# Kernel tuning notes

Hardware: AMD Instinct MI355X
Metric: run time of the kernel (lower is better)

The kernel has to match this reference:

```python
import jax, jax.numpy as jnp
import numpy as np

EPS = 1e-5


def _layer_norm(x, gamma, beta):
    mu = jnp.mean(x, axis=-1, keepdims=True)
    var = jnp.var(x, axis=-1, keepdims=True)
    return (x - mu) * jax.lax.rsqrt(var + EPS) * gamma + beta


def setup_inputs() -> dict:
    key = jax.random.key(0)
    B, I, H = 4096, 1024, 1024
    ks = jax.random.split(key, 6)
    x = jax.random.normal(ks[0], (B, I), dtype=jnp.float32)
    h = jax.random.normal(ks[1], (B, H), dtype=jnp.float32)
    c = jax.random.normal(ks[2], (B, H), dtype=jnp.float32)
    # nn.Linear(I+H, 4H): weight [4H, I+H], bias [4H]
    bound = 1.0 / np.sqrt(I + H)
    W = jax.random.uniform(ks[3], (4 * H, I + H), minval=-bound, maxval=bound, dtype=jnp.float32)
    b = jax.random.uniform(ks[4], (4 * H,), minval=-bound, maxval=bound, dtype=jnp.float32)
    inp = {"x": x, "h": h, "c": c, "W": W, "b": b}
    for name in ("i", "f", "g", "o", "c"):
        inp[f"ln_{name}_g"] = jnp.ones((H,), dtype=jnp.float32)
        inp[f"ln_{name}_b"] = jnp.zeros((H,), dtype=jnp.float32)
    return inp


def reference(x, h, c, W, b, ln_i_g, ln_i_b, ln_f_g, ln_f_b, ln_g_g, ln_g_b,
              ln_o_g, ln_o_b, ln_c_g, ln_c_b):
    H = h.shape[-1]
    xh = jnp.concatenate([x, h], axis=-1)              # [B, I+H]
    gates = xh @ W.T + b                               # [B, 4H]
    i_raw, f_raw, g_raw, o_raw = jnp.split(gates, 4, axis=-1)
    i = jax.nn.sigmoid(_layer_norm(i_raw, ln_i_g, ln_i_b))
    f = jax.nn.sigmoid(_layer_norm(f_raw, ln_f_g, ln_f_b))
    g = jnp.tanh(_layer_norm(g_raw, ln_g_g, ln_g_b))
    o = jax.nn.sigmoid(_layer_norm(o_raw, ln_o_g, ln_o_b))
    c_new = f * c + i * g
    h_new = o * jnp.tanh(_layer_norm(c_new, ln_c_g, ln_c_b))
    return (h_new, c_new)
```

## Files before the change

kernel.cpp:

```cpp
#include <hip/hip_runtime.h>
#include <hip/hip_bf16.h>

#define B_ROWS 4096
#define H_DIM  1024
#define K_DIM  2048
#define N_DIM  4096
#define NT32   64

typedef __attribute__((ext_vector_type(8))) short bf16x8;
typedef __attribute__((ext_vector_type(16))) float f32x16;

__device__ __forceinline__ unsigned short f2bf(float f) {
  union { float f; unsigned int u; } v; v.f = f;
  unsigned int u = v.u;
  return (unsigned short)((u + 0x7fffu + ((u >> 16) & 1u)) >> 16);
}
__device__ __forceinline__ float bf2f(unsigned short u) {
  union { unsigned int u; float f; } v; v.u = ((unsigned int)u) << 16;
  return v.f;
}

__device__ __forceinline__ void gload_lds16(const void* g, void* l) {
  __builtin_amdgcn_global_load_lds(
      (const __attribute__((address_space(1))) void*)g,
      (__attribute__((address_space(3))) void*)l, 16, 0, 0);
}

__global__ __launch_bounds__(256) void pack_kernel(
    const float* __restrict__ x, const float* __restrict__ h,
    const float* __restrict__ W, unsigned short* __restrict__ Abf,
    unsigned short* __restrict__ Wbf) {
  int bid = blockIdx.x;
  if (bid < 8192) {
    int t = bid * 256 + threadIdx.x;
    int e = t * 4;
    int row = e >> 11;
    int col = e & 2047;
    const float* src = (col < 1024) ? (x + (size_t)row * 1024 + col)
                                    : (h + (size_t)row * 1024 + (col - 1024));
    float4 v = *(const float4*)src;
    ushort4 o;
    o.x = f2bf(v.x); o.y = f2bf(v.y); o.z = f2bf(v.z); o.w = f2bf(v.w);
    *(ushort4*)(Abf + e) = o;
  } else {
    int t = (bid - 8192) * 256 + threadIdx.x;
    int e = t * 4;
    float4 v = *(const float4*)(W + e);
    ushort4 o;
    o.x = f2bf(v.x); o.y = f2bf(v.y); o.z = f2bf(v.z); o.w = f2bf(v.w);
    *(ushort4*)(Wbf + e) = o;
  }
}


#define UNR _Pragma("unroll")

#define PSTG(kt, BUFOFS)                                                     \
  {                                                                          \
    const size_t ko = (size_t)(kt) << 5;                                     \
    char* const Ld = lds + (BUFOFS);                                         \
    gload_lds16(gAw0 + ko, Ld + dstOfs);                                     \
    gload_lds16(gAw1 + ko, Ld + dstOfs + 1024);                              \
    gload_lds16(gBw0 + ko, Ld + 16384 + dstOfs);                             \
    gload_lds16(gBw1 + ko, Ld + 16384 + dstOfs + 1024);                      \
  }

#define TILE1(tt, BUF, FRa, FRb, FWa, FWb)                                   \
  {                                                                          \
    const int kt3 = ((tt) + 3) & (NT32 - 1);                                 \
    PSTG(kt3, (((BUF) + 3) & 3) * 32768);                                    \
    asm volatile("s_waitcnt vmcnt(8)" ::: "memory");                         \
    __builtin_amdgcn_s_barrier();                                            \
    const char* const Ln = lds + (((BUF) + 1) & 3) * 32768;                  \
    UNR for (int R = 0; R < 4; ++R) {                                        \
      FWa[R][0] = *(const bf16x8*)(Ln + (wm * 8 + 2 * R) * 1024 + lofs0);    \
      FWa[R][1] = *(const bf16x8*)(Ln + (wm * 8 + 2 * R) * 1024 + lofs1);    \
    }                                                                        \
    UNR for (int ni = 0; ni < 2; ++ni) {                                     \
      FWb[ni][0] = *(const bf16x8*)(Ln + 16384 +                             \
                                    (wn * 4 + 2 * ni) * 1024 + lofs0);       \
      FWb[ni][1] = *(const bf16x8*)(Ln + 16384 +                             \
                                    (wn * 4 + 2 * ni) * 1024 + lofs1);       \
    }                                                                        \
    asm volatile("s_waitcnt lgkmcnt(12)" ::: "memory");                      \
    __builtin_amdgcn_sched_barrier(0);                                       \
    __builtin_amdgcn_s_setprio(1);                                           \
    UNR for (int R = 0; R < 4; ++R)                                          \
      UNR for (int ni = 0; ni < 2; ++ni)                                     \
        UNR for (int h = 0; h < 2; ++h)                                      \
          acc[R][ni] = __builtin_amdgcn_mfma_f32_32x32x16_bf16(              \
              FRa[R][h], FRb[ni][h], acc[R][ni], 0, 0, 0);                   \
    __builtin_amdgcn_s_setprio(0);                                           \
  }

__global__ __launch_bounds__(512, 2) void gemm_kernel(
    const unsigned short* __restrict__ A, const unsigned short* __restrict__ W,
    const float* __restrict__ bias, unsigned short* __restrict__ C) {
  __shared__ __align__(16) char lds[131072];

  const int tid = threadIdx.x;
  const int w = tid >> 6, l = tid & 63;
  const int wm = w >> 2, wn = w & 3;

  const int bid = blockIdx.x;
  const int xcd = bid & 7, li = bid >> 3;
  const int by = (xcd & 3) * 4 + (li >> 3);
  const int bx = ((xcd >> 2) << 3) + (li & 7);
  const int bm = by * 256, bn = bx * 256;

  const int lofs0 = ((l >> 4) & 1) * 1024 + (l & 15) * 64 +
                    ((((l >> 5) * 16) ^ ((l & 8) << 2)) ^ (((l >> 4) & 1) << 4));
  const int lofs1 = lofs0 ^ 32;

  const int lane_r = (l >> 2) & 15;
  const int lane_c0 = ((l & 3) * 8) ^ (((l >> 5) & 1) * 16);
  const int lane_c1 = lane_c0 ^ 8;

  const int dstOfs = w * 2048;
  const unsigned short* gAw0 = A + (size_t)(bm + 32 * w + lane_r) * K_DIM + lane_c0;
  const unsigned short* gAw1 = A + (size_t)(bm + 32 * w + 16 + lane_r) * K_DIM + lane_c1;
  const unsigned short* gBw0 = W + (size_t)(bn + 32 * w + lane_r) * K_DIM + lane_c0;
  const unsigned short* gBw1 = W + (size_t)(bn + 32 * w + 16 + lane_r) * K_DIM + lane_c1;

  f32x16 acc[4][2];
#pragma unroll
  for (int i = 0; i < 4; ++i)
#pragma unroll
    for (int j = 0; j < 2; ++j) acc[i][j] = (f32x16)0.0f;

  PSTG(0, 0);
  PSTG(1, 32768);
  PSTG(2, 65536);
  asm volatile("s_waitcnt vmcnt(8)" ::: "memory");
  __builtin_amdgcn_s_barrier();

  bf16x8 aP[4][2], bP[2][2], aQ[4][2], bQ[2][2];
#pragma unroll
  for (int R = 0; R < 4; ++R) {
    aP[R][0] = *(const bf16x8*)(lds + (wm * 8 + 2 * R) * 1024 + lofs0);
    aP[R][1] = *(const bf16x8*)(lds + (wm * 8 + 2 * R) * 1024 + lofs1);
  }
#pragma unroll
  for (int ni = 0; ni < 2; ++ni) {
    bP[ni][0] = *(const bf16x8*)(lds + 16384 + (wn * 4 + 2 * ni) * 1024 + lofs0);
    bP[ni][1] = *(const bf16x8*)(lds + 16384 + (wn * 4 + 2 * ni) * 1024 + lofs1);
  }

  for (int t = 0; t < NT32; t += 4) {
    TILE1(t + 0, 0, aP, bP, aQ, bQ);
    TILE1(t + 1, 1, aQ, bQ, aP, bP);
    TILE1(t + 2, 2, aP, bP, aQ, bQ);
    TILE1(t + 3, 3, aQ, bQ, aP, bP);
  }

  const int cl = l & 31, hi = l >> 5;
  float bv[2];
#pragma unroll
  for (int ni = 0; ni < 2; ++ni) bv[ni] = bias[bn + wn * 64 + ni * 32 + cl];
  unsigned short* Cb = C + (size_t)(bm + wm * 128) * N_DIM + bn + wn * 64;
#pragma unroll
  for (int R = 0; R < 4; ++R)
#pragma unroll
    for (int ni = 0; ni < 2; ++ni)
#pragma unroll
      for (int r = 0; r < 16; ++r) {
        const int row = R * 32 + (r & 3) + 8 * (r >> 2) + 4 * hi;
        Cb[(size_t)row * N_DIM + ni * 32 + cl] = f2bf(acc[R][ni][r] + bv[ni]);
      }
}

__device__ __forceinline__ float sigmoidf_(float x) {
  return 1.0f / (1.0f + __expf(-x));
}
__device__ __forceinline__ float tanhf_(float x) {
  return 1.0f - 2.0f / (__expf(2.0f * x) + 1.0f);
}

__global__ __launch_bounds__(256) void ln_lstm_kernel(
    const unsigned short* __restrict__ gates, const float* __restrict__ cprev,
    const float* __restrict__ g_i, const float* __restrict__ b_i,
    const float* __restrict__ g_f, const float* __restrict__ b_f,
    const float* __restrict__ g_g, const float* __restrict__ b_g,
    const float* __restrict__ g_o, const float* __restrict__ b_o,
    const float* __restrict__ g_c, const float* __restrict__ b_c,
    float* __restrict__ out) {
  const int b = blockIdx.x;
  const int t = threadIdx.x;
  const int wid = t >> 6, lane = t & 63;
  __shared__ float red[32];

  const unsigned short* grow = gates + (size_t)b * N_DIM;
  const int c0 = t * 4;

  float v[4][4];
#pragma unroll
  for (int g = 0; g < 4; g++) {
    ushort4 raw = *(const ushort4*)(grow + g * 1024 + c0);
    v[g][0] = bf2f(raw.x); v[g][1] = bf2f(raw.y);
    v[g][2] = bf2f(raw.z); v[g][3] = bf2f(raw.w);
  }

  const float4 gamma[4] = {*(const float4*)(g_i + c0), *(const float4*)(g_f + c0),
                           *(const float4*)(g_g + c0), *(const float4*)(g_o + c0)};
  const float4 beta[4]  = {*(const float4*)(b_i + c0), *(const float4*)(b_f + c0),
                           *(const float4*)(b_g + c0), *(const float4*)(b_o + c0)};

  float s[8];
#pragma unroll
  for (int g = 0; g < 4; g++) {
    s[g]     = v[g][0] + v[g][1] + v[g][2] + v[g][3];
    s[4 + g] = v[g][0]*v[g][0] + v[g][1]*v[g][1] + v[g][2]*v[g][2] + v[g][3]*v[g][3];
  }
#pragma unroll
  for (int o = 32; o >= 1; o >>= 1)
#pragma unroll
    for (int i = 0; i < 8; i++) s[i] += __shfl_xor(s[i], o, 64);
  if (lane == 0) {
#pragma unroll
    for (int i = 0; i < 8; i++) red[wid * 8 + i] = s[i];
  }
  __syncthreads();
#pragma unroll
  for (int i = 0; i < 8; i++) s[i] = red[i] + red[8 + i] + red[16 + i] + red[24 + i];

  float a[4][4];
#pragma unroll
  for (int g = 0; g < 4; g++) {
    float mu = s[g] * (1.0f / 1024.0f);
    float var = s[4 + g] * (1.0f / 1024.0f) - mu * mu;
    float inv = rsqrtf(var + 1e-5f);
    const float* gm = (const float*)&gamma[g];
    const float* bt = (const float*)&beta[g];
#pragma unroll
    for (int j = 0; j < 4; j++) {
      float n = (v[g][j] - mu) * inv * gm[j] + bt[j];
      a[g][j] = (g == 2) ? tanhf_(n) : sigmoidf_(n);
    }
  }

  float4 cp = *(const float4*)(cprev + (size_t)b * 1024 + c0);
  const float* cpe = (const float*)&cp;
  float cn[4];
#pragma unroll
  for (int j = 0; j < 4; j++)
    cn[j] = a[1][j] * cpe[j] + a[0][j] * a[2][j];

  {
    float u0 = cn[0] + cn[1] + cn[2] + cn[3];
    float u1 = cn[0]*cn[0] + cn[1]*cn[1] + cn[2]*cn[2] + cn[3]*cn[3];
#pragma unroll
    for (int o = 32; o >= 1; o >>= 1) {
      u0 += __shfl_xor(u0, o, 64);
      u1 += __shfl_xor(u1, o, 64);
    }
    __syncthreads();
    if (lane == 0) { red[wid * 2] = u0; red[wid * 2 + 1] = u1; }
    __syncthreads();
    u0 = red[0] + red[2] + red[4] + red[6];
    u1 = red[1] + red[3] + red[5] + red[7];
    float mu = u0 * (1.0f / 1024.0f);
    float var = u1 * (1.0f / 1024.0f) - mu * mu;
    float inv = rsqrtf(var + 1e-5f);
    float4 gm = *(const float4*)(g_c + c0);
    float4 bt = *(const float4*)(b_c + c0);
    const float* gme = (const float*)&gm;
    const float* bte = (const float*)&bt;
    float hn[4];
#pragma unroll
    for (int j = 0; j < 4; j++) {
      float n = (cn[j] - mu) * inv * gme[j] + bte[j];
      hn[j] = a[3][j] * tanhf_(n);
    }
    *(float4*)(out + (size_t)b * 1024 + c0) = make_float4(hn[0], hn[1], hn[2], hn[3]);
    *(float4*)(out + (size_t)B_ROWS * H_DIM + (size_t)b * 1024 + c0) =
        make_float4(cn[0], cn[1], cn[2], cn[3]);
  }
}

extern "C" void kernel_launch(void* const* d_in, const int* in_sizes, int n_in,
                              void* d_out, int out_size, void* d_ws,
                              size_t ws_size, hipStream_t stream) {
  const float* x    = (const float*)d_in[0];
  const float* h    = (const float*)d_in[1];
  const float* c    = (const float*)d_in[2];
  const float* W    = (const float*)d_in[3];
  const float* bias = (const float*)d_in[4];
  const float* ln_i_g = (const float*)d_in[5];
  const float* ln_i_b = (const float*)d_in[6];
  const float* ln_f_g = (const float*)d_in[7];
  const float* ln_f_b = (const float*)d_in[8];
  const float* ln_g_g = (const float*)d_in[9];
  const float* ln_g_b = (const float*)d_in[10];
  const float* ln_o_g = (const float*)d_in[11];
  const float* ln_o_b = (const float*)d_in[12];
  const float* ln_c_g = (const float*)d_in[13];
  const float* ln_c_b = (const float*)d_in[14];

  unsigned short* Abf = (unsigned short*)d_ws;
  unsigned short* Wbf = Abf + (size_t)B_ROWS * K_DIM;
  unsigned short* gates = Wbf + (size_t)N_DIM * K_DIM;

  pack_kernel<<<16384, 256, 0, stream>>>(x, h, W, Abf, Wbf);

  dim3 ggrid(256);
  gemm_kernel<<<ggrid, 512, 0, stream>>>(Abf, Wbf, bias, gates);

  ln_lstm_kernel<<<B_ROWS, 256, 0, stream>>>(
      gates, c, ln_i_g, ln_i_b, ln_f_g, ln_f_b, ln_g_g, ln_g_b,
      ln_o_g, ln_o_b, ln_c_g, ln_c_b, (float*)d_out);
}
```

Before: 111.0 us.

## Switch GEMM to 16x16x32 MFMA with 16 waves and two-stage prefetch

Restructures the GEMM to use 1024-thread blocks of 16 waves in a 4x4 grid. Each wave computes a 64x64 sub-tile with 16x16x32 bf16 MFMAs instead of 128x64 with 32x32x16. The prefetch depth drops from three tiles ahead to two, and the register double-buffering of LDS fragments is removed: fragments are loaded and fully waited on within each tile. This aims to raise wave-level parallelism for latency hiding, but loses the LDS-read/MFMA overlap and lowers per-wave data reuse. The __launch_bounds__(1024, 4) hint cannot be met with 128 KB of shared memory per block.

```diff
diff --git a/kernel.cpp b/kernel.cpp
--- a/kernel.cpp
+++ b/kernel.cpp
@@ -8,7 +8,7 @@
 #define NT32   64
 
 typedef __attribute__((ext_vector_type(8))) short bf16x8;
-typedef __attribute__((ext_vector_type(16))) float f32x16;
+typedef __attribute__((ext_vector_type(4))) float f32x4;
 
 __device__ __forceinline__ unsigned short f2bf(float f) {
   union { float f; unsigned int u; } v; v.f = f;
@@ -59,41 +59,33 @@
   {                                                                          \
     const size_t ko = (size_t)(kt) << 5;                                     \
     char* const Ld = lds + (BUFOFS);                                         \
-    gload_lds16(gAw0 + ko, Ld + dstOfs);                                     \
-    gload_lds16(gAw1 + ko, Ld + dstOfs + 1024);                              \
-    gload_lds16(gBw0 + ko, Ld + 16384 + dstOfs);                             \
-    gload_lds16(gBw1 + ko, Ld + 16384 + dstOfs + 1024);                      \
-  }
-
-#define TILE1(tt, BUF, FRa, FRb, FWa, FWb)                                   \
+    gload_lds16(gAw + ko, Ld + dstOfs);                                      \
+    gload_lds16(gBw + ko, Ld + 16384 + dstOfs);                              \
+  }
+
+#define TILE1(tt, BUF)                                                       \
   {                                                                          \
-    const int kt3 = ((tt) + 3) & (NT32 - 1);                                 \
-    PSTG(kt3, (((BUF) + 3) & 3) * 32768);                                    \
-    asm volatile("s_waitcnt vmcnt(8)" ::: "memory");                         \
+    const int kt2 = ((tt) + 2) & (NT32 - 1);                                 \
+    PSTG(kt2, (((BUF) + 2) & 3) * 32768);                                    \
+    asm volatile("s_waitcnt vmcnt(2)" ::: "memory");                         \
     __builtin_amdgcn_s_barrier();                                            \
-    const char* const Ln = lds + (((BUF) + 1) & 3) * 32768;                  \
-    UNR for (int R = 0; R < 4; ++R) {                                        \
-      FWa[R][0] = *(const bf16x8*)(Ln + (wm * 8 + 2 * R) * 1024 + lofs0);    \
-      FWa[R][1] = *(const bf16x8*)(Ln + (wm * 8 + 2 * R) * 1024 + lofs1);    \
-    }                                                                        \
-    UNR for (int ni = 0; ni < 2; ++ni) {                                     \
-      FWb[ni][0] = *(const bf16x8*)(Ln + 16384 +                             \
-                                    (wn * 4 + 2 * ni) * 1024 + lofs0);       \
-      FWb[ni][1] = *(const bf16x8*)(Ln + 16384 +                             \
-                                    (wn * 4 + 2 * ni) * 1024 + lofs1);       \
-    }                                                                        \
-    asm volatile("s_waitcnt lgkmcnt(12)" ::: "memory");                      \
+    const char* const Lc = lds + (BUF) * 32768;                              \
+    bf16x8 aF[4], bF[4];                                                     \
+    UNR for (int mi = 0; mi < 4; ++mi)                                       \
+      aF[mi] = *(const bf16x8*)(Lc + (wm * 4 + mi) * 1024 + lofs);           \
+    UNR for (int ni = 0; ni < 4; ++ni)                                       \
+      bF[ni] = *(const bf16x8*)(Lc + 16384 + (wn * 4 + ni) * 1024 + lofs);   \
+    asm volatile("s_waitcnt lgkmcnt(0)" ::: "memory");                       \
     __builtin_amdgcn_sched_barrier(0);                                       \
     __builtin_amdgcn_s_setprio(1);                                           \
-    UNR for (int R = 0; R < 4; ++R)                                          \
-      UNR for (int ni = 0; ni < 2; ++ni)                                     \
-        UNR for (int h = 0; h < 2; ++h)                                      \
-          acc[R][ni] = __builtin_amdgcn_mfma_f32_32x32x16_bf16(              \
-              FRa[R][h], FRb[ni][h], acc[R][ni], 0, 0, 0);                   \
+    UNR for (int mi = 0; mi < 4; ++mi)                                       \
+      UNR for (int ni = 0; ni < 4; ++ni)                                     \
+        acc[mi][ni] = __builtin_amdgcn_mfma_f32_16x16x32_bf16(               \
+            aF[mi], bF[ni], acc[mi][ni], 0, 0, 0);                           \
     __builtin_amdgcn_s_setprio(0);                                           \
   }
 
-__global__ __launch_bounds__(512, 2) void gemm_kernel(
+__global__ __launch_bounds__(1024, 4) void gemm_kernel(
     const unsigned short* __restrict__ A, const unsigned short* __restrict__ W,
     const float* __restrict__ bias, unsigned short* __restrict__ C) {
   __shared__ __align__(16) char lds[131072];
@@ -108,65 +100,44 @@
   const int bx = ((xcd >> 2) << 3) + (li & 7);
   const int bm = by * 256, bn = bx * 256;
 
-  const int lofs0 = ((l >> 4) & 1) * 1024 + (l & 15) * 64 +
-                    ((((l >> 5) * 16) ^ ((l & 8) << 2)) ^ (((l >> 4) & 1) << 4));
-  const int lofs1 = lofs0 ^ 32;
-
+  const int lofs = (((l & 15) * 64) + ((l >> 4) * 16)) ^ ((l & 8) << 2);
   const int lane_r = (l >> 2) & 15;
-  const int lane_c0 = ((l & 3) * 8) ^ (((l >> 5) & 1) * 16);
-  const int lane_c1 = lane_c0 ^ 8;
-
-  const int dstOfs = w * 2048;
-  const unsigned short* gAw0 = A + (size_t)(bm + 32 * w + lane_r) * K_DIM + lane_c0;
-  const unsigned short* gAw1 = A + (size_t)(bm + 32 * w + 16 + lane_r) * K_DIM + lane_c1;
-  const unsigned short* gBw0 = W + (size_t)(bn + 32 * w + lane_r) * K_DIM + lane_c0;
-  const unsigned short* gBw1 = W + (size_t)(bn + 32 * w + 16 + lane_r) * K_DIM + lane_c1;
-
-  f32x16 acc[4][2];
+  const int lane_c = ((l & 3) * 8) ^ (((l >> 5) & 1) * 16);
+
+  const int dstOfs = w * 1024;
+  const unsigned short* gAw = A + (size_t)(bm + 16 * w + lane_r) * K_DIM + lane_c;
+  const unsigned short* gBw = W + (size_t)(bn + 16 * w + lane_r) * K_DIM + lane_c;
+
+  f32x4 acc[4][4];
 #pragma unroll
   for (int i = 0; i < 4; ++i)
 #pragma unroll
-    for (int j = 0; j < 2; ++j) acc[i][j] = (f32x16)0.0f;
+    for (int j = 0; j < 4; ++j) acc[i][j] = (f32x4)0.0f;
 
   PSTG(0, 0);
   PSTG(1, 32768);
-  PSTG(2, 65536);
-  asm volatile("s_waitcnt vmcnt(8)" ::: "memory");
-  __builtin_amdgcn_s_barrier();
-
-  bf16x8 aP[4][2], bP[2][2], aQ[4][2], bQ[2][2];
-#pragma unroll
-  for (int R = 0; R < 4; ++R) {
-    aP[R][0] = *(const bf16x8*)(lds + (wm * 8 + 2 * R) * 1024 + lofs0);
-    aP[R][1] = *(const bf16x8*)(lds + (wm * 8 + 2 * R) * 1024 + lofs1);
-  }
-#pragma unroll
-  for (int ni = 0; ni < 2; ++ni) {
-    bP[ni][0] = *(const bf16x8*)(lds + 16384 + (wn * 4 + 2 * ni) * 1024 + lofs0);
-    bP[ni][1] = *(const bf16x8*)(lds + 16384 + (wn * 4 + 2 * ni) * 1024 + lofs1);
-  }
 
   for (int t = 0; t < NT32; t += 4) {
-    TILE1(t + 0, 0, aP, bP, aQ, bQ);
-    TILE1(t + 1, 1, aQ, bQ, aP, bP);
-    TILE1(t + 2, 2, aP, bP, aQ, bQ);
-    TILE1(t + 3, 3, aQ, bQ, aP, bP);
-  }
-
-  const int cl = l & 31, hi = l >> 5;
-  float bv[2];
-#pragma unroll
-  for (int ni = 0; ni < 2; ++ni) bv[ni] = bias[bn + wn * 64 + ni * 32 + cl];
-  unsigned short* Cb = C + (size_t)(bm + wm * 128) * N_DIM + bn + wn * 64;
-#pragma unroll
-  for (int R = 0; R < 4; ++R)
-#pragma unroll
-    for (int ni = 0; ni < 2; ++ni)
-#pragma unroll
-      for (int r = 0; r < 16; ++r) {
-        const int row = R * 32 + (r & 3) + 8 * (r >> 2) + 4 * hi;
-        Cb[(size_t)row * N_DIM + ni * 32 + cl] = f2bf(acc[R][ni][r] + bv[ni]);
-      }
+    TILE1(t + 0, 0);
+    TILE1(t + 1, 1);
+    TILE1(t + 2, 2);
+    TILE1(t + 3, 3);
+  }
+
+  const int lm = l & 15, lq = l >> 4;
+  float bv[4];
+#pragma unroll
+  for (int ni = 0; ni < 4; ++ni) bv[ni] = bias[bn + wn * 64 + ni * 16 + lm];
+  unsigned short* Cb = C + (size_t)(bm + wm * 64) * N_DIM + bn + wn * 64;
+#pragma unroll
+  for (int mi = 0; mi < 4; ++mi)
+#pragma unroll
+    for (int j = 0; j < 4; ++j) {
+      const size_t rofs = (size_t)(mi * 16 + lq * 4 + j) * N_DIM;
+#pragma unroll
+      for (int ni = 0; ni < 4; ++ni)
+        Cb[rofs + ni * 16 + lm] = f2bf(acc[mi][ni][j] + bv[ni]);
+    }
 }
 
 __device__ __forceinline__ float sigmoidf_(float x) {
@@ -303,7 +274,7 @@
   pack_kernel<<<16384, 256, 0, stream>>>(x, h, W, Abf, Wbf);
 
   dim3 ggrid(256);
-  gemm_kernel<<<ggrid, 512, 0, stream>>>(Abf, Wbf, bias, gates);
+  gemm_kernel<<<ggrid, 1024, 0, stream>>>(Abf, Wbf, bias, gates);
 
   ln_lstm_kernel<<<B_ROWS, 256, 0, stream>>>(
       gates, c, ln_i_g, ln_i_b, ln_f_g, ln_f_b, ln_g_g, ln_g_b,
```

New measurement: 106.3 us. 1.04x faster.
